# Kernel tuning notes

Hardware: AMD Instinct MI355X
Metric: run time of the kernel (lower is better)

The kernel has to match this reference:

```python
import jax, jax.numpy as jnp
import numpy as np

NS, NV = 16, 4          # scalar / vector multiplicities
MODES = 2               # spectral conv retained fourier modes
C_OUT = 40              # out irreps dim: 16 + 4*3 + 4*3
EPS = 1e-5


def setup_inputs() -> dict:
    key = jax.random.key(0)
    ks = jax.random.split(key, 10)
    T, N, E = 8, 10000, 32768
    x = jax.random.normal(ks[0], (T, N, 28), jnp.float32)
    edge_index = jax.random.randint(ks[1], (2, E), 0, N)
    edge_attr = jax.random.normal(ks[2], (T, E, 48), jnp.float32)
    edge_sh = jax.random.normal(ks[3], (T, E, 4), jnp.float32)
    s = 1.0 / np.sqrt(48.0)
    w_mlp1 = jax.random.normal(ks[4], (48, 48), jnp.float32) * s
    b_mlp1 = jnp.zeros((48,), jnp.float32)
    w_mlp2 = jax.random.normal(ks[5], (48, 416), jnp.float32) * s
    b_mlp2 = jnp.zeros((416,), jnp.float32)
    sc = 1.0 / (NS * NS)
    tc_wr = jax.random.uniform(ks[6], (NS, NS, MODES), jnp.float32) * sc
    tc_wi = jax.random.uniform(ks[7], (NS, NS, MODES), jnp.float32) * sc
    bn_gamma = jnp.ones((C_OUT,), jnp.float32)
    bn_beta = jnp.zeros((C_OUT,), jnp.float32)
    return dict(x=x, edge_index=edge_index, edge_attr=edge_attr, edge_sh=edge_sh,
                w_mlp1=w_mlp1, b_mlp1=b_mlp1, w_mlp2=w_mlp2, b_mlp2=b_mlp2,
                tc_wr=tc_wr, tc_wi=tc_wi, bn_gamma=bn_gamma, bn_beta=bn_beta)


def reference(x, edge_index, edge_attr, edge_sh,
              w_mlp1, b_mlp1, w_mlp2, b_mlp2,
              tc_wr, tc_wi, bn_gamma, bn_beta):
    T, N, _ = x.shape
    E = edge_index.shape[1]
    src, dst = edge_index[0], edge_index[1]

    # ---- SpectralConv1d over the time axis (scalar channels only) ----
    xs = x[:, :, :NS]                                   # [T,N,16]
    xf = jnp.fft.rfft(xs, axis=0)                       # [T//2+1,N,16] c64
    w = tc_wr + 1j * tc_wi                              # [16,16,M]
    low = jnp.einsum('tni,iom->tno', xf[:MODES], jnp.moveaxis(w, -1, 0).transpose(1, 2, 0)[..., :MODES]) if False else jnp.einsum('mni,iom->mno', xf[:MODES], w)
    out_ft = jnp.zeros((T // 2 + 1, N, NS), jnp.complex64).at[:MODES].set(low)
    x_scalar = jnp.fft.irfft(out_ft, n=T, axis=0)       # [T,N,16]

    # ---- edge MLP -> per-edge tensor-product weights [T,E,416] ----
    h = jax.nn.relu(edge_attr @ w_mlp1 + b_mlp1)
    ew = h @ w_mlp2 + b_mlp2

    # ---- gather source node features per edge ----
    xe = x[:, src]                                      # [T,E,28]
    s = xe[..., :NS]                                    # [T,E,16]
    v = xe[..., NS:].reshape(T, E, NV, 3)               # [T,E,4,3]
    sh0 = edge_sh[..., :1]                              # [T,E,1]
    sh1 = edge_sh[..., 1:4]                             # [T,E,3]

    # path weight splits: 0e*0e->0e | 0e*1o->1o | 1o*0e->1o | 1o*1o->0e | 1o*1o->1e
    w00 = ew[..., 0:256].reshape(T, E, NS, NS)
    w01 = ew[..., 256:320].reshape(T, E, NS, NV)
    w10 = ew[..., 320:336].reshape(T, E, NV, NV)
    w110 = ew[..., 336:400].reshape(T, E, NV, NS)
    w111 = ew[..., 400:416].reshape(T, E, NV, NV)

    inv3 = 1.0 / np.sqrt(3.0)
    inv6 = 1.0 / np.sqrt(6.0)
    n0 = 1.0 / np.sqrt(20.0)   # fan-in norm for 0e output (16 + 4 paths)
    n1o = 1.0 / np.sqrt(20.0)  # fan-in norm for 1o output (16 + 4 paths)
    n1e = 1.0 / np.sqrt(4.0)   # fan-in norm for 1e output

    # scalar outputs
    p1 = jnp.einsum('tei,teio->teo', s * sh0, w00)
    vdots = jnp.einsum('teid,ted->tei', v, sh1) * inv3
    p4 = jnp.einsum('tei,teio->teo', vdots, w110)
    out0 = (p1 + p4) * n0                               # [T,E,16]

    # odd-vector outputs
    p2 = jnp.einsum('tei,teio->teo', s, w01)[..., None] * sh1[:, :, None, :] * inv3
    p3 = jnp.einsum('teid,teio->teod', v * sh0[..., None], w10) * inv3
    out1o = (p2 + p3) * n1o                             # [T,E,4,3]

    c = jnp.cross(v, sh1[:, :, None, :]) * inv6
    out1e = jnp.einsum('teid,teio->teod', c, w111) * n1e  # [T,E,4,3]

    msg = jnp.concatenate([out0,
                           out1o.reshape(T, E, NV * 3),
                           out1e.reshape(T, E, NV * 3)], axis=-1)  # [T,E,40]

    # ---- scatter_mean over destination nodes ----
    seg = jax.vmap(lambda m: jax.ops.segment_sum(m, dst, num_segments=N))(msg)
    cnt = jax.ops.segment_sum(jnp.ones((E,), msg.dtype), dst, num_segments=N)
    y = seg / jnp.maximum(cnt, 1.0)[None, :, None]      # [T,N,40]

    # ---- add spectral time-conv result to scalar channels ----
    y = jnp.concatenate([y[..., :NS] + x_scalar, y[..., NS:]], axis=-1)

    # ---- BatchNorm1d replicating torch permute/reshape semantics ----
    z = jnp.transpose(y, (1, 2, 0)).reshape(-1, C_OUT)  # [N*T, 40] (torch layout)
    mu = z.mean(axis=0)
    var = z.var(axis=0)
    z = (z - mu) / jnp.sqrt(var + EPS) * bn_gamma + bn_beta
    y = jnp.transpose(z.reshape(N, C_OUT, T), (2, 0, 1))
    return y
```

## Files before the change

### kernel.cpp

```cpp
#include <hip/hip_runtime.h>
#include <math.h>

#define TT 8
#define NN 10000
#define EE 32768
#define CC 40
#define EPSV 1e-05f

constexpr float INV3 = 0.57735026918962576f;
constexpr float INV6 = 0.40824829046386302f;
constexpr float N0F  = 0.22360679774997896f;
constexpr float N1OF = 0.22360679774997896f;
constexpr float N1EF = 0.5f;

constexpr float CTab[8] = {1.f, 0.70710678118654752f, 0.f, -0.70710678118654752f,
                           -1.f, -0.70710678118654752f, 0.f, 0.70710678118654752f};
constexpr float STab[8] = {0.f, 0.70710678118654752f, 1.f, 0.70710678118654752f,
                           0.f, -0.70710678118654752f, -1.f, -0.70710678118654752f};

typedef __attribute__((ext_vector_type(8))) short short8;
typedef __attribute__((ext_vector_type(4))) float f32x4;

__device__ __forceinline__ void atomAdd(float* p, float v) {
  __hip_atomic_fetch_add(p, v, __ATOMIC_RELAXED, __HIP_MEMORY_SCOPE_AGENT);
}

__device__ __forceinline__ short f2bfs(float f) {
  unsigned u = __builtin_bit_cast(unsigned, f);
  u = (u + 0x7fffu + ((u >> 16) & 1u)) >> 16;
  return (short)u;
}
__device__ __forceinline__ float bf2f(ushort u) {
  unsigned v = ((unsigned)u) << 16;
  return __builtin_bit_cast(float, v);
}

#define SPEC_B 157
#define PREP_B 116
__global__ __launch_bounds__(256) void k_pre(const float* __restrict__ x,
                                             const float* __restrict__ wr,
                                             const float* __restrict__ wi,
                                             const float* __restrict__ W1,
                                             const float* __restrict__ W2,
                                             float* __restrict__ xsc,
                                             short* __restrict__ W1F,
                                             short* __restrict__ W2F) {
  int b = blockIdx.x, tid = threadIdx.x;
  if (b < SPEC_B) {
    int gid = b * 256 + tid;
    int n = gid >> 2, og = gid & 3;
    if (n >= NN) return;
    float F0[16], A[16], B[16];
#pragma unroll
    for (int i = 0; i < 16; ++i) { F0[i] = 0.f; A[i] = 0.f; B[i] = 0.f; }
#pragma unroll
    for (int t = 0; t < 8; ++t) {
      const float4* xp = (const float4*)(x + ((size_t)t * NN + n) * 28);
      float4 v0 = xp[0], v1 = xp[1], v2 = xp[2], v3 = xp[3];
      const float ct = CTab[t], st = STab[t];
      float vv[16] = {v0.x, v0.y, v0.z, v0.w, v1.x, v1.y, v1.z, v1.w,
                      v2.x, v2.y, v2.z, v2.w, v3.x, v3.y, v3.z, v3.w};
#pragma unroll
      for (int i = 0; i < 16; ++i) {
        F0[i] += vv[i];
        A[i] = fmaf(vv[i], ct, A[i]);
        B[i] = fmaf(vv[i], -st, B[i]);
      }
    }
#pragma unroll
    for (int oo = 0; oo < 4; ++oo) {
      int o = og * 4 + oo;
      float r0 = 0.f, r1 = 0.f, i1 = 0.f;
#pragma unroll
      for (int i = 0; i < 16; ++i) {
        float wr0 = wr[i * 32 + o * 2 + 0];
        float wr1 = wr[i * 32 + o * 2 + 1];
        float wi1 = wi[i * 32 + o * 2 + 1];
        r0 = fmaf(F0[i], wr0, r0);
        r1 += A[i] * wr1 - B[i] * wi1;
        i1 += A[i] * wi1 + B[i] * wr1;
      }
#pragma unroll
      for (int t = 0; t < 8; ++t) {
        float val = 0.125f * (r0 + 2.f * (r1 * CTab[t] - i1 * STab[t]));
        xsc[((size_t)t * NN + n) * 16 + o] = val;
      }
    }
  } else {
    int idx = (b - SPEC_B) * 256 + tid;
    const int tot1 = 3 * 2 * 64 * 8;
    if (idx < tot1) {
      int elem = idx & 7, lane = (idx >> 3) & 63, kt = (idx >> 9) & 1, nt = idx >> 10;
      int j = kt * 32 + ((lane >> 4) << 2) + (elem & 3) + ((elem >> 2) << 4);
      int n = nt * 16 + (lane & 15);
      W1F[idx] = (j < 48) ? f2bfs(W1[j * 48 + n]) : (short)0;
    } else {
      int id2 = idx - tot1;
      int elem = id2 & 7, lane = (id2 >> 3) & 63, kt = (id2 >> 9) & 1, ck = id2 >> 10;
      int j = kt * 32 + ((lane >> 4) << 2) + (elem & 3) + ((elem >> 2) << 4);
      int n = ck * 16 + (lane & 15);
      W2F[id2] = (j < 48) ? f2bfs(W2[j * 416 + n]) : (short)0;
    }
  }
}

__global__ __launch_bounds__(1024) void k_scanbucket(const int* __restrict__ ei,
                                                     int* __restrict__ row_start,
                                                     int* __restrict__ ipos,
                                                     float* __restrict__ stats) {
  __shared__ int lcnt[NN];
  __shared__ int wtot[16];
  __shared__ int wpre[16];
  int tid = threadIdx.x;
  if (tid < 80) stats[tid] = 0.f;
  for (int i = tid; i < NN; i += 1024) lcnt[i] = 0;
  __syncthreads();
#pragma unroll
  for (int it = 0; it < EE / 1024; ++it) {
    int e = it * 1024 + tid;
    atomicAdd(&lcnt[ei[EE + e]], 1);
  }
  __syncthreads();
  const int PER = 10;
  int base = tid * PER;
  int s = 0;
  if (base < NN) {
#pragma unroll
    for (int i = 0; i < PER; ++i) s += lcnt[base + i];
  }
  int incl = s;
  int lane = tid & 63, wid = tid >> 6;
#pragma unroll
  for (int off = 1; off < 64; off <<= 1) {
    int v = __shfl_up(incl, off);
    if (lane >= off) incl += v;
  }
  if (lane == 63) wtot[wid] = incl;
  __syncthreads();
  if (tid == 0) {
    int run = 0;
#pragma unroll
    for (int i = 0; i < 16; ++i) { wpre[i] = run; run += wtot[i]; }
  }
  __syncthreads();
  int run = wpre[wid] + (incl - s);
  if (base < NN) {
#pragma unroll
    for (int i = 0; i < PER; ++i) {
      int n = base + i;
      int d = lcnt[n];
      row_start[n] = run;
      lcnt[n] = run;
      run += d;
    }
  }
  if (tid == 0) row_start[NN] = EE;
  __syncthreads();
#pragma unroll
  for (int it = 0; it < EE / 1024; ++it) {
    int e = it * 1024 + tid;
    int d = ei[EE + e];
    int slot = atomicAdd(&lcnt[d], 1);
    ipos[e] = slot;
  }
}

__global__ __launch_bounds__(256) void k_edge4(
    const float* __restrict__ x,
    const int* __restrict__ ei,
    const float* __restrict__ eag,
    const float* __restrict__ shg,
    const short* __restrict__ W1F,
    const short* __restrict__ W2F,
    const float* __restrict__ b1,
    const float* __restrict__ b2,
    const int* __restrict__ ipos,
    ushort* __restrict__ msg)
{
  __shared__ float cSs[16][64];
  __shared__ float rawSs[16][64];
  __shared__ float cVDs[4][64];
  __shared__ float vS0s[12][64];
  __shared__ float sh1fs[3][64];
  __shared__ float cCRs[12][64];
  __shared__ int   iposs[64];
  __shared__ ushort Hs[4][16][64];

  int blk = blockIdx.x;
  int t = blk >> 9;
  int e0 = (blk & 511) * 64;
  int tid = threadIdx.x;

  {
    int e = tid & 63;
    int role = tid >> 6;
    int eg = e0 + e;
    const float* shp = shg + ((size_t)t * EE + eg) * 4;
    float sh0 = shp[0], s1x = shp[1], s1y = shp[2], s1z = shp[3];
    int src = ei[eg];
    const float* xr = x + ((size_t)t * NN + src) * 28;
    const float F1 = INV3 * N1OF;
    if (role == 0) {
      iposs[e] = ipos[eg];
      sh1fs[0][e] = s1x * F1; sh1fs[1][e] = s1y * F1; sh1fs[2][e] = s1z * F1;
#pragma unroll
      for (int i = 0; i < 8; ++i) {
        float s = xr[i];
        rawSs[i][e] = s;
        cSs[i][e] = s * sh0 * N0F;
      }
    } else if (role == 1) {
#pragma unroll
      for (int i = 8; i < 16; ++i) {
        float s = xr[i];
        rawSs[i][e] = s;
        cSs[i][e] = s * sh0 * N0F;
      }
    } else {
      int i0 = (role == 2) ? 0 : 2;
#pragma unroll
      for (int ii = 0; ii < 2; ++ii) {
        int i = i0 + ii;
        float vx = xr[16 + 3 * i], vy = xr[17 + 3 * i], vz = xr[18 + 3 * i];
        cVDs[i][e] = (vx * s1x + vy * s1y + vz * s1z) * INV3 * N0F;
        vS0s[3 * i + 0][e] = vx * sh0 * F1;
        vS0s[3 * i + 1][e] = vy * sh0 * F1;
        vS0s[3 * i + 2][e] = vz * sh0 * F1;
        cCRs[3 * i + 0][e] = (vy * s1z - vz * s1y) * INV6 * N1EF;
        cCRs[3 * i + 1][e] = (vz * s1x - vx * s1z) * INV6 * N1EF;
        cCRs[3 * i + 2][e] = (vx * s1y - vy * s1x) * INV6 * N1EF;
      }
    }
  }
  __syncthreads();

  int w = tid >> 6, l = tid & 63;
  int col = l & 15;
  int kq  = (l >> 4) << 2;
  int eb  = w * 16;

  const float* row = eag + ((size_t)t * EE + e0 + eb + col) * 48;
  float4 fa = *(const float4*)(row + kq);
  float4 fb = *(const float4*)(row + 16 + kq);
  float4 fc = *(const float4*)(row + 32 + kq);
  short8 a0, a1;
  a0[0] = f2bfs(fa.x); a0[1] = f2bfs(fa.y); a0[2] = f2bfs(fa.z); a0[3] = f2bfs(fa.w);
  a0[4] = f2bfs(fb.x); a0[5] = f2bfs(fb.y); a0[6] = f2bfs(fb.z); a0[7] = f2bfs(fb.w);
  a1[0] = f2bfs(fc.x); a1[1] = f2bfs(fc.y); a1[2] = f2bfs(fc.z); a1[3] = f2bfs(fc.w);
  a1[4] = 0; a1[5] = 0; a1[6] = 0; a1[7] = 0;

  const short8* w1f = (const short8*)W1F;
  const short8* w2f = (const short8*)W2F;

#pragma unroll
  for (int nt = 0; nt < 3; ++nt) {
    float bias = b1[nt * 16 + col];
    f32x4 c = {bias, bias, bias, bias};
    c = __builtin_amdgcn_mfma_f32_16x16x32_bf16(a0, w1f[(nt * 2 + 0) * 64 + l], c, 0, 0, 0);
    c = __builtin_amdgcn_mfma_f32_16x16x32_bf16(a1, w1f[(nt * 2 + 1) * 64 + l], c, 0, 0, 0);
#pragma unroll
    for (int r = 0; r < 4; ++r) {
      int m = kq + r;
      float hv = fmaxf(c[r], 0.f);
      Hs[w][m][(nt * 16 + col) ^ ((m & 7) << 3)] = (ushort)f2bfs(hv);
    }
  }
#pragma unroll
  for (int r = 0; r < 4; ++r) {
    int m = kq + r;
    Hs[w][m][(48 + col) ^ ((m & 7) << 3)] = 0;
  }

  int m2 = col, X = (m2 & 7) << 3;
  ushort4 r0 = *(const ushort4*)&Hs[w][m2][(kq +  0) ^ X];
  ushort4 r1 = *(const ushort4*)&Hs[w][m2][(kq + 16) ^ X];
  ushort4 r2 = *(const ushort4*)&Hs[w][m2][(kq + 32) ^ X];
  ushort4 r3 = *(const ushort4*)&Hs[w][m2][(kq + 48) ^ X];
  short8 A20, A21;
  A20[0] = (short)r0.x; A20[1] = (short)r0.y; A20[2] = (short)r0.z; A20[3] = (short)r0.w;
  A20[4] = (short)r1.x; A20[5] = (short)r1.y; A20[6] = (short)r1.z; A20[7] = (short)r1.w;
  A21[0] = (short)r2.x; A21[1] = (short)r2.y; A21[2] = (short)r2.z; A21[3] = (short)r2.w;
  A21[4] = (short)r3.x; A21[5] = (short)r3.y; A21[6] = (short)r3.z; A21[7] = (short)r3.w;

  float acc0[4]  = {0.f, 0.f, 0.f, 0.f};
  float accP2[4] = {0.f, 0.f, 0.f, 0.f};
  float acc1o[3][4] = {{0.f,0.f,0.f,0.f},{0.f,0.f,0.f,0.f},{0.f,0.f,0.f,0.f}};
  float acc1e[3][4] = {{0.f,0.f,0.f,0.f},{0.f,0.f,0.f,0.f},{0.f,0.f,0.f,0.f}};
  int er0 = eb + kq;
  int iloc = col >> 2;
  int o = col & 3;

  short8 pf0[4], pf1[4];
#pragma unroll
  for (int i = 0; i < 4; ++i) {
    pf0[i] = w2f[(2 * i + 0) * 64 + l];
    pf1[i] = w2f[(2 * i + 1) * 64 + l];
  }

#pragma unroll
  for (int ck = 0; ck < 26; ++ck) {
    short8 B0 = pf0[ck & 3], B1 = pf1[ck & 3];
    if (ck + 4 < 26) {
      pf0[ck & 3] = w2f[(2 * (ck + 4) + 0) * 64 + l];
      pf1[ck & 3] = w2f[(2 * (ck + 4) + 1) * 64 + l];
    }
    float bias = b2[ck * 16 + col];
    f32x4 c = {bias, bias, bias, bias};
    c = __builtin_amdgcn_mfma_f32_16x16x32_bf16(A20, B0, c, 0, 0, 0);
    c = __builtin_amdgcn_mfma_f32_16x16x32_bf16(A21, B1, c, 0, 0, 0);

    if (ck < 16) {
#pragma unroll
      for (int r = 0; r < 4; ++r)
        acc0[r] = fmaf(cSs[ck][er0 + r], c[r], acc0[r]);
    } else if (ck < 20) {
#pragma unroll
      for (int r = 0; r < 4; ++r) {
        float q = rawSs[(ck - 16) * 4 + iloc][er0 + r] * c[r];
        q += __shfl_xor(q, 4);
        q += __shfl_xor(q, 8);
        accP2[r] += q;
      }
    } else if (ck == 20) {
#pragma unroll
      for (int d = 0; d < 3; ++d)
#pragma unroll
        for (int r = 0; r < 4; ++r) {
          float q = vS0s[iloc * 3 + d][er0 + r] * c[r];
          q += __shfl_xor(q, 4);
          q += __shfl_xor(q, 8);
          acc1o[d][r] += q;
        }
    } else if (ck < 25) {
#pragma unroll
      for (int r = 0; r < 4; ++r)
        acc0[r] = fmaf(cVDs[ck - 21][er0 + r], c[r], acc0[r]);
    } else {
#pragma unroll
      for (int d = 0; d < 3; ++d)
#pragma unroll
        for (int r = 0; r < 4; ++r) {
          float q = cCRs[iloc * 3 + d][er0 + r] * c[r];
          q += __shfl_xor(q, 4);
          q += __shfl_xor(q, 8);
          acc1e[d][r] += q;
        }
    }
  }

#pragma unroll
  for (int r = 0; r < 4; ++r) {
    size_t eg = (size_t)t * EE + iposs[er0 + r];
    msg[eg * 40 + col] = (ushort)f2bfs(acc0[r]);
  }
  if (col < 4) {
#pragma unroll
    for (int r = 0; r < 4; ++r) {
      int e = er0 + r;
      size_t eg = (size_t)t * EE + iposs[e];
      ushort* mrow = msg + eg * 40;
#pragma unroll
      for (int d = 0; d < 3; ++d) {
        mrow[16 + 3 * o + d] = (ushort)f2bfs(fmaf(accP2[r], sh1fs[d][e], acc1o[d][r]));
        mrow[28 + 3 * o + d] = (ushort)f2bfs(acc1e[d][r]);
      }
    }
  }
}

__global__ __launch_bounds__(320) void k_gstats(const ushort* __restrict__ msg,
                                                const int* __restrict__ row_start,
                                                const float* __restrict__ xsc,
                                                float* __restrict__ out,
                                                float* __restrict__ stats) {
  int blk = blockIdx.x;
  int t = blk / 157;
  int nb = blk - t * 157;
  int tid = threadIdx.x;
  int g = tid / 40, c = tid - g * 40;
  int r5 = c % 5;
  __shared__ float sred[10];
  if (tid < 10) sred[tid] = 0.f;
  __syncthreads();
  float p = 0.f, q = 0.f;
  for (int step = 0; step < 8; ++step) {
    int n = nb * 64 + step * 8 + g;
    if (n < NN) {
      int a = row_start[n], b = row_start[n + 1];
      float acc = 0.f;
      for (int j = a; j < b; ++j)
        acc += bf2f(msg[((size_t)t * EE + j) * 40 + c]);
      float y = acc / fmaxf((float)(b - a), 1.f) +
                (c < 16 ? xsc[((size_t)t * NN + n) * 16 + c] : 0.f);
      out[((size_t)t * NN + n) * 40 + c] = y;
      p += y;
      q = fmaf(y, y, q);
    }
  }
  atomicAdd(&sred[r5], p);
  atomicAdd(&sred[5 + r5], q);
  __syncthreads();
  if (tid < 10) {
    int r = tid % 5;
    int j = 8 * r + t;
    atomAdd(stats + (tid >= 5 ? 40 + j : j), sred[tid]);
  }
}

__global__ __launch_bounds__(256) void k_norm(const float* __restrict__ stats,
                                              const float* __restrict__ gam,
                                              const float* __restrict__ bet,
                                              float* __restrict__ out) {
  int idx4 = blockIdx.x * 256 + threadIdx.x;
  if (idx4 >= TT * NN * 10) return;
  int t = idx4 / (NN * 10);
  int rem = idx4 - t * NN * 10;
  int c0 = (rem % 10) * 4;
  const float inv = 1.f / (8.f * (float)NN);
  float4* op = (float4*)out;
  float4 y = op[idx4];
  float vals[4] = {y.x, y.y, y.z, y.w};
#pragma unroll
  for (int k = 0; k < 4; ++k) {
    int c = c0 + k;
    int j = 8 * (c % 5) + t;
    float mu = stats[j] * inv;
    float var = stats[40 + j] * inv - mu * mu;
    vals[k] = (vals[k] - mu) * rsqrtf(var + EPSV) * gam[j] + bet[j];
  }
  y.x = vals[0]; y.y = vals[1]; y.z = vals[2]; y.w = vals[3];
  op[idx4] = y;
}

extern "C" void kernel_launch(void* const* d_in, const int* in_sizes, int n_in,
                              void* d_out, int out_size, void* d_ws, size_t ws_size,
                              hipStream_t stream) {
  const float* x   = (const float*)d_in[0];
  const int*   ei  = (const int*)d_in[1];
  const float* ea  = (const float*)d_in[2];
  const float* esh = (const float*)d_in[3];
  const float* W1  = (const float*)d_in[4];
  const float* b1  = (const float*)d_in[5];
  const float* W2  = (const float*)d_in[6];
  const float* b2  = (const float*)d_in[7];
  const float* wr  = (const float*)d_in[8];
  const float* wi  = (const float*)d_in[9];
  const float* gam = (const float*)d_in[10];
  const float* bet = (const float*)d_in[11];
  float* out = (float*)d_out;

  float*  xsc       = (float*)d_ws;
  ushort* W1F       = (ushort*)(xsc + 1280000);
  ushort* W2F       = W1F + 3072;
  ushort* msg       = W2F + 26624;
  float*  stats     = (float*)(msg + (size_t)10485760);
  int*    row_start = (int*)(stats + 80);
  int*    ipos      = row_start + 10001;

  k_pre<<<SPEC_B + PREP_B, 256, 0, stream>>>(x, wr, wi, W1, W2, xsc,
                                             (short*)W1F, (short*)W2F);
  k_scanbucket<<<1, 1024, 0, stream>>>(ei, row_start, ipos, stats);
  k_edge4<<<TT * (EE / 64), 256, 0, stream>>>(x, ei, ea, esh, (short*)W1F, (short*)W2F,
                                              b1, b2, ipos, msg);
  k_gstats<<<TT * 157, 320, 0, stream>>>(msg, row_start, xsc, out, stats);
  k_norm<<<(TT * NN * 10 + 255) / 256, 256, 0, stream>>>(stats, gam, bet, out);
}
```

Measured before the change: 146.4 us.

## Fold scan-bucket into prep kernel and process two edge tiles per wave

The single-block CSR scan/bucket kernel is merged into block 0 of the prep kernel, now with 256 threads instead of 1024, which removes one launch and lets the scan overlap with the spectral and weight-packing work. The edge kernel drops to 128 threads per block and each wave handles two 16-edge tiles. This reuses each loaded W1/W2 B-fragment across two MFMAs and halves the waves that issue weight loads. The cost is more registers per thread, a larger Hs buffer per wave, and a slower serial scan in block 0, which may now be the longest block of the prep kernel.

Result: slower. 166.4 us (+13.7%).

```diff
diff --git a/kernel.cpp b/kernel.cpp
--- a/kernel.cpp
+++ b/kernel.cpp
@@ -40,14 +40,70 @@
 __global__ __launch_bounds__(256) void k_pre(const float* __restrict__ x,
                                              const float* __restrict__ wr,
                                              const float* __restrict__ wi,
+                                             const int* __restrict__ ei,
                                              const float* __restrict__ W1,
                                              const float* __restrict__ W2,
                                              float* __restrict__ xsc,
                                              short* __restrict__ W1F,
-                                             short* __restrict__ W2F) {
+                                             short* __restrict__ W2F,
+                                             int* __restrict__ row_start,
+                                             int* __restrict__ ipos,
+                                             float* __restrict__ stats) {
+  __shared__ int lcnt[NN];
+  __shared__ int wtot[4];
+  __shared__ int wpre[4];
   int b = blockIdx.x, tid = threadIdx.x;
-  if (b < SPEC_B) {
-    int gid = b * 256 + tid;
+  if (b == 0) {
+    if (tid < 80) stats[tid] = 0.f;
+    for (int i = tid; i < NN; i += 256) lcnt[i] = 0;
+    __syncthreads();
+    for (int it = 0; it < EE / 256; ++it) {
+      int e = it * 256 + tid;
+      atomicAdd(&lcnt[ei[EE + e]], 1);
+    }
+    __syncthreads();
+    const int PER = 40;
+    int base = tid * PER;
+    int s = 0;
+    for (int i = 0; i < PER; ++i) {
+      int idx = base + i;
+      if (idx < NN) s += lcnt[idx];
+    }
+    int incl = s;
+    int lane = tid & 63, wid = tid >> 6;
+#pragma unroll
+    for (int off = 1; off < 64; off <<= 1) {
+      int v = __shfl_up(incl, off);
+      if (lane >= off) incl += v;
+    }
+    if (lane == 63) wtot[wid] = incl;
+    __syncthreads();
+    if (tid == 0) {
+      int run = 0;
+#pragma unroll
+      for (int i = 0; i < 4; ++i) { wpre[i] = run; run += wtot[i]; }
+    }
+    __syncthreads();
+    int run = wpre[wid] + (incl - s);
+    for (int i = 0; i < PER; ++i) {
+      int idx = base + i;
+      if (idx < NN) {
+        int d = lcnt[idx];
+        row_start[idx] = run;
+        lcnt[idx] = run;
+        run += d;
+      }
+    }
+    if (tid == 0) row_start[NN] = EE;
+    __syncthreads();
+    for (int it = 0; it < EE / 256; ++it) {
+      int e = it * 256 + tid;
+      int d = ei[EE + e];
+      int slot = atomicAdd(&lcnt[d], 1);
+      ipos[e] = slot;
+    }
+  } else if (b <= SPEC_B) {
+    int gid = (b - 1) * 256 + tid;
     int n = gid >> 2, og = gid & 3;
     if (n >= NN) return;
     float F0[16], A[16], B[16];
@@ -87,7 +143,7 @@
       }
     }
   } else {
-    int idx = (b - SPEC_B) * 256 + tid;
+    int idx = (b - 1 - SPEC_B) * 256 + tid;
     const int tot1 = 3 * 2 * 64 * 8;
     if (idx < tot1) {
       int elem = idx & 7, lane = (idx >> 3) & 63, kt = (idx >> 9) & 1, nt = idx >> 10;
@@ -104,68 +160,7 @@
   }
 }
 
-__global__ __launch_bounds__(1024) void k_scanbucket(const int* __restrict__ ei,
-                                                     int* __restrict__ row_start,
-                                                     int* __restrict__ ipos,
-                                                     float* __restrict__ stats) {
-  __shared__ int lcnt[NN];
-  __shared__ int wtot[16];
-  __shared__ int wpre[16];
-  int tid = threadIdx.x;
-  if (tid < 80) stats[tid] = 0.f;
-  for (int i = tid; i < NN; i += 1024) lcnt[i] = 0;
-  __syncthreads();
-#pragma unroll
-  for (int it = 0; it < EE / 1024; ++it) {
-    int e = it * 1024 + tid;
-    atomicAdd(&lcnt[ei[EE + e]], 1);
-  }
-  __syncthreads();
-  const int PER = 10;
-  int base = tid * PER;
-  int s = 0;
-  if (base < NN) {
-#pragma unroll
-    for (int i = 0; i < PER; ++i) s += lcnt[base + i];
-  }
-  int incl = s;
-  int lane = tid & 63, wid = tid >> 6;
-#pragma unroll
-  for (int off = 1; off < 64; off <<= 1) {
-    int v = __shfl_up(incl, off);
-    if (lane >= off) incl += v;
-  }
-  if (lane == 63) wtot[wid] = incl;
-  __syncthreads();
-  if (tid == 0) {
-    int run = 0;
-#pragma unroll
-    for (int i = 0; i < 16; ++i) { wpre[i] = run; run += wtot[i]; }
-  }
-  __syncthreads();
-  int run = wpre[wid] + (incl - s);
-  if (base < NN) {
-#pragma unroll
-    for (int i = 0; i < PER; ++i) {
-      int n = base + i;
-      int d = lcnt[n];
-      row_start[n] = run;
-      lcnt[n] = run;
-      run += d;
-    }
-  }
-  if (tid == 0) row_start[NN] = EE;
-  __syncthreads();
-#pragma unroll
-  for (int it = 0; it < EE / 1024; ++it) {
-    int e = it * 1024 + tid;
-    int d = ei[EE + e];
-    int slot = atomicAdd(&lcnt[d], 1);
-    ipos[e] = slot;
-  }
-}
-
-__global__ __launch_bounds__(256) void k_edge4(
+__global__ __launch_bounds__(128, 3) void k_edge2t(
     const float* __restrict__ x,
     const int* __restrict__ ei,
     const float* __restrict__ eag,
@@ -184,7 +179,7 @@
   __shared__ float sh1fs[3][64];
   __shared__ float cCRs[12][64];
   __shared__ int   iposs[64];
-  __shared__ ushort Hs[4][16][64];
+  __shared__ ushort Hs[2][2][16][64];
 
   int blk = blockIdx.x;
   int t = blk >> 9;
@@ -204,23 +199,14 @@
       iposs[e] = ipos[eg];
       sh1fs[0][e] = s1x * F1; sh1fs[1][e] = s1y * F1; sh1fs[2][e] = s1z * F1;
 #pragma unroll
-      for (int i = 0; i < 8; ++i) {
+      for (int i = 0; i < 16; ++i) {
         float s = xr[i];
         rawSs[i][e] = s;
         cSs[i][e] = s * sh0 * N0F;
       }
-    } else if (role == 1) {
-#pragma unroll
-      for (int i = 8; i < 16; ++i) {
-        float s = xr[i];
-        rawSs[i][e] = s;
-        cSs[i][e] = s * sh0 * N0F;
-      }
     } else {
-      int i0 = (role == 2) ? 0 : 2;
-#pragma unroll
-      for (int ii = 0; ii < 2; ++ii) {
-        int i = i0 + ii;
+#pragma unroll
+      for (int i = 0; i < 4; ++i) {
         float vx = xr[16 + 3 * i], vy = xr[17 + 3 * i], vz = xr[18 + 3 * i];
         cVDs[i][e] = (vx * s1x + vy * s1y + vz * s1z) * INV3 * N0F;
         vS0s[3 * i + 0][e] = vx * sh0 * F1;
@@ -237,17 +223,26 @@
   int w = tid >> 6, l = tid & 63;
   int col = l & 15;
   int kq  = (l >> 4) << 2;
-  int eb  = w * 16;
-
-  const float* row = eag + ((size_t)t * EE + e0 + eb + col) * 48;
-  float4 fa = *(const float4*)(row + kq);
-  float4 fb = *(const float4*)(row + 16 + kq);
-  float4 fc = *(const float4*)(row + 32 + kq);
-  short8 a0, a1;
-  a0[0] = f2bfs(fa.x); a0[1] = f2bfs(fa.y); a0[2] = f2bfs(fa.z); a0[3] = f2bfs(fa.w);
-  a0[4] = f2bfs(fb.x); a0[5] = f2bfs(fb.y); a0[6] = f2bfs(fb.z); a0[7] = f2bfs(fb.w);
-  a1[0] = f2bfs(fc.x); a1[1] = f2bfs(fc.y); a1[2] = f2bfs(fc.z); a1[3] = f2bfs(fc.w);
-  a1[4] = 0; a1[5] = 0; a1[6] = 0; a1[7] = 0;
+  int ebA = w * 32;
+  int ebB = w * 32 + 16;
+
+  const float* rowA = eag + ((size_t)t * EE + e0 + ebA + col) * 48;
+  const float* rowB = eag + ((size_t)t * EE + e0 + ebB + col) * 48;
+  float4 fa = *(const float4*)(rowA + kq);
+  float4 fb = *(const float4*)(rowA + 16 + kq);
+  float4 fc = *(const float4*)(rowA + 32 + kq);
+  float4 ga = *(const float4*)(rowB + kq);
+  float4 gb = *(const float4*)(rowB + 16 + kq);
+  float4 gc = *(const float4*)(rowB + 32 + kq);
+  short8 a0A, a1A, a0B, a1B;
+  a0A[0] = f2bfs(fa.x); a0A[1] = f2bfs(fa.y); a0A[2] = f2bfs(fa.z); a0A[3] = f2bfs(fa.w);
+  a0A[4] = f2bfs(fb.x); a0A[5] = f2bfs(fb.y); a0A[6] = f2bfs(fb.z); a0A[7] = f2bfs(fb.w);
+  a1A[0] = f2bfs(fc.x); a1A[1] = f2bfs(fc.y); a1A[2] = f2bfs(fc.z); a1A[3] = f2bfs(fc.w);
+  a1A[4] = 0; a1A[5] = 0; a1A[6] = 0; a1A[7] = 0;
+  a0B[0] = f2bfs(ga.x); a0B[1] = f2bfs(ga.y); a0B[2] = f2bfs(ga.z); a0B[3] = f2bfs(ga.w);
+  a0B[4] = f2bfs(gb.x); a0B[5] = f2bfs(gb.y); a0B[6] = f2bfs(gb.z); a0B[7] = f2bfs(gb.w);
+  a1B[0] = f2bfs(gc.x); a1B[1] = f2bfs(gc.y); a1B[2] = f2bfs(gc.z); a1B[3] = f2bfs(gc.w);
+  a1B[4] = 0; a1B[5] = 0; a1B[6] = 0; a1B[7] = 0;
 
   const short8* w1f = (const short8*)W1F;
   const short8* w2f = (const short8*)W2F;
@@ -255,38 +250,60 @@
 #pragma unroll
   for (int nt = 0; nt < 3; ++nt) {
     float bias = b1[nt * 16 + col];
-    f32x4 c = {bias, bias, bias, bias};
-    c = __builtin_amdgcn_mfma_f32_16x16x32_bf16(a0, w1f[(nt * 2 + 0) * 64 + l], c, 0, 0, 0);
-    c = __builtin_amdgcn_mfma_f32_16x16x32_bf16(a1, w1f[(nt * 2 + 1) * 64 + l], c, 0, 0, 0);
+    short8 wb0 = w1f[(nt * 2 + 0) * 64 + l];
+    short8 wb1 = w1f[(nt * 2 + 1) * 64 + l];
+    f32x4 cA = {bias, bias, bias, bias};
+    cA = __builtin_amdgcn_mfma_f32_16x16x32_bf16(a0A, wb0, cA, 0, 0, 0);
+    cA = __builtin_amdgcn_mfma_f32_16x16x32_bf16(a1A, wb1, cA, 0, 0, 0);
+    f32x4 cB = {bias, bias, bias, bias};
+    cB = __builtin_amdgcn_mfma_f32_16x16x32_bf16(a0B, wb0, cB, 0, 0, 0);
+    cB = __builtin_amdgcn_mfma_f32_16x16x32_bf16(a1B, wb1, cB, 0, 0, 0);
 #pragma unroll
     for (int r = 0; r < 4; ++r) {
       int m = kq + r;
-      float hv = fmaxf(c[r], 0.f);
-      Hs[w][m][(nt * 16 + col) ^ ((m & 7) << 3)] = (ushort)f2bfs(hv);
+      int cidx = (nt * 16 + col) ^ ((m & 7) << 3);
+      Hs[w][0][m][cidx] = (ushort)f2bfs(fmaxf(cA[r], 0.f));
+      Hs[w][1][m][cidx] = (ushort)f2bfs(fmaxf(cB[r], 0.f));
     }
   }
 #pragma unroll
   for (int r = 0; r < 4; ++r) {
     int m = kq + r;
-    Hs[w][m][(48 + col) ^ ((m & 7) << 3)] = 0;
+    int cidx = (48 + col) ^ ((m & 7) << 3);
+    Hs[w][0][m][cidx] = 0;
+    Hs[w][1][m][cidx] = 0;
   }
 
   int m2 = col, X = (m2 & 7) << 3;
-  ushort4 r0 = *(const ushort4*)&Hs[w][m2][(kq +  0) ^ X];
-  ushort4 r1 = *(const ushort4*)&Hs[w][m2][(kq + 16) ^ X];
-  ushort4 r2 = *(const ushort4*)&Hs[w][m2][(kq + 32) ^ X];
-  ushort4 r3 = *(const ushort4*)&Hs[w][m2][(kq + 48) ^ X];
-  short8 A20, A21;
-  A20[0] = (short)r0.x; A20[1] = (short)r0.y; A20[2] = (short)r0.z; A20[3] = (short)r0.w;
-  A20[4] = (short)r1.x; A20[5] = (short)r1.y; A20[6] = (short)r1.z; A20[7] = (short)r1.w;
-  A21[0] = (short)r2.x; A21[1] = (short)r2.y; A21[2] = (short)r2.z; A21[3] = (short)r2.w;
-  A21[4] = (short)r3.x; A21[5] = (short)r3.y; A21[6] = (short)r3.z; A21[7] = (short)r3.w;
-
-  float acc0[4]  = {0.f, 0.f, 0.f, 0.f};
-  float accP2[4] = {0.f, 0.f, 0.f, 0.f};
-  float acc1o[3][4] = {{0.f,0.f,0.f,0.f},{0.f,0.f,0.f,0.f},{0.f,0.f,0.f,0.f}};
-  float acc1e[3][4] = {{0.f,0.f,0.f,0.f},{0.f,0.f,0.f,0.f},{0.f,0.f,0.f,0.f}};
-  int er0 = eb + kq;
+  short8 A20A, A21A, A20B, A21B;
+  {
+    ushort4 r0 = *(const ushort4*)&Hs[w][0][m2][(kq +  0) ^ X];
+    ushort4 r1 = *(const ushort4*)&Hs[w][0][m2][(kq + 16) ^ X];
+    ushort4 r2 = *(const ushort4*)&Hs[w][0][m2][(kq + 32) ^ X];
+    ushort4 r3 = *(const ushort4*)&Hs[w][0][m2][(kq + 48) ^ X];
+    A20A[0] = (short)r0.x; A20A[1] = (short)r0.y; A20A[2] = (short)r0.z; A20A[3] = (short)r0.w;
+    A20A[4] = (short)r1.x; A20A[5] = (short)r1.y; A20A[6] = (short)r1.z; A20A[7] = (short)r1.w;
+    A21A[0] = (short)r2.x; A21A[1] = (short)r2.y; A21A[2] = (short)r2.z; A21A[3] = (short)r2.w;
+    A21A[4] = (short)r3.x; A21A[5] = (short)r3.y; A21A[6] = (short)r3.z; A21A[7] = (short)r3.w;
+  }
+  {
+    ushort4 r0 = *(const ushort4*)&Hs[w][1][m2][(kq +  0) ^ X];
+    ushort4 r1 = *(const ushort4*)&Hs[w][1][m2][(kq + 16) ^ X];
+    ushort4 r2 = *(const ushort4*)&Hs[w][1][m2][(kq + 32) ^ X];
+    ushort4 r3 = *(const ushort4*)&Hs[w][1][m2][(kq + 48) ^ X];
+    A20B[0] = (short)r0.x; A20B[1] = (short)r0.y; A20B[2] = (short)r0.z; A20B[3] = (short)r0.w;
+    A20B[4] = (short)r1.x; A20B[5] = (short)r1.y; A20B[6] = (short)r1.z; A20B[7] = (short)r1.w;
+    A21B[0] = (short)r2.x; A21B[1] = (short)r2.y; A21B[2] = (short)r2.z; A21B[3] = (short)r2.w;
+    A21B[4] = (short)r3.x; A21B[5] = (short)r3.y; A21B[6] = (short)r3.z; A21B[7] = (short)r3.w;
+  }
+
+  float acc0[2][4]  = {{0.f,0.f,0.f,0.f},{0.f,0.f,0.f,0.f}};
+  float accP2[2][4] = {{0.f,0.f,0.f,0.f},{0.f,0.f,0.f,0.f}};
+  float acc1o[2][3][4] = {{{0.f,0.f,0.f,0.f},{0.f,0.f,0.f,0.f},{0.f,0.f,0.f,0.f}},
+                          {{0.f,0.f,0.f,0.f},{0.f,0.f,0.f,0.f},{0.f,0.f,0.f,0.f}}};
+  float acc1e[2][3][4] = {{{0.f,0.f,0.f,0.f},{0.f,0.f,0.f,0.f},{0.f,0.f,0.f,0.f}},
+                          {{0.f,0.f,0.f,0.f},{0.f,0.f,0.f,0.f},{0.f,0.f,0.f,0.f}}};
+  int er[2] = {ebA + kq, ebB + kq};
   int iloc = col >> 2;
   int o = col & 3;
 
@@ -305,64 +322,77 @@
       pf1[ck & 3] = w2f[(2 * (ck + 4) + 1) * 64 + l];
     }
     float bias = b2[ck * 16 + col];
-    f32x4 c = {bias, bias, bias, bias};
-    c = __builtin_amdgcn_mfma_f32_16x16x32_bf16(A20, B0, c, 0, 0, 0);
-    c = __builtin_amdgcn_mfma_f32_16x16x32_bf16(A21, B1, c, 0, 0, 0);
-
-    if (ck < 16) {
-#pragma unroll
-      for (int r = 0; r < 4; ++r)
-        acc0[r] = fmaf(cSs[ck][er0 + r], c[r], acc0[r]);
-    } else if (ck < 20) {
-#pragma unroll
-      for (int r = 0; r < 4; ++r) {
-        float q = rawSs[(ck - 16) * 4 + iloc][er0 + r] * c[r];
-        q += __shfl_xor(q, 4);
-        q += __shfl_xor(q, 8);
-        accP2[r] += q;
-      }
-    } else if (ck == 20) {
-#pragma unroll
-      for (int d = 0; d < 3; ++d)
+    f32x4 cc0 = {bias, bias, bias, bias};
+    cc0 = __builtin_amdgcn_mfma_f32_16x16x32_bf16(A20A, B0, cc0, 0, 0, 0);
+    cc0 = __builtin_amdgcn_mfma_f32_16x16x32_bf16(A21A, B1, cc0, 0, 0, 0);
+    f32x4 cc1 = {bias, bias, bias, bias};
+    cc1 = __builtin_amdgcn_mfma_f32_16x16x32_bf16(A20B, B0, cc1, 0, 0, 0);
+    cc1 = __builtin_amdgcn_mfma_f32_16x16x32_bf16(A21B, B1, cc1, 0, 0, 0);
+    f32x4 cc[2] = {cc0, cc1};
+
+#pragma unroll
+    for (int tb = 0; tb < 2; ++tb) {
+      if (ck < 16) {
+#pragma unroll
+        for (int r = 0; r < 4; ++r)
+          acc0[tb][r] = fmaf(cSs[ck][er[tb] + r], cc[tb][r], acc0[tb][r]);
+      } else if (ck < 20) {
 #pragma unroll
         for (int r = 0; r < 4; ++r) {
-          float q = vS0s[iloc * 3 + d][er0 + r] * c[r];
+          float q = rawSs[(ck - 16) * 4 + iloc][er[tb] + r] * cc[tb][r];
           q += __shfl_xor(q, 4);
           q += __shfl_xor(q, 8);
-          acc1o[d][r] += q;
+          accP2[tb][r] += q;
         }
-    } else if (ck < 25) {
-#pragma unroll
-      for (int r = 0; r < 4; ++r)
-        acc0[r] = fmaf(cVDs[ck - 21][er0 + r], c[r], acc0[r]);
-    } else {
-#pragma unroll
-      for (int d = 0; d < 3; ++d)
-#pragma unroll
-        for (int r = 0; r < 4; ++r) {
-          float q = cCRs[iloc * 3 + d][er0 + r] * c[r];
-          q += __shfl_xor(q, 4);
-          q += __shfl_xor(q, 8);
-          acc1e[d][r] += q;
+      } else if (ck == 20) {
+#pragma unroll
+        for (int d = 0; d < 3; ++d)
+#pragma unroll
+          for (int r = 0; r < 4; ++r) {
+            float q = vS0s[iloc * 3 + d][er[tb] + r] * cc[tb][r];
+            q += __shfl_xor(q, 4);
+            q += __shfl_xor(q, 8);
+            acc1o[tb][d][r] += q;
+          }
+      } else if (ck < 25) {
+#pragma unroll
+        for (int r = 0; r < 4; ++r)
+          acc0[tb][r] = fmaf(cVDs[ck - 21][er[tb] + r], cc[tb][r], acc0[tb][r]);
+      } else {
+#pragma unroll
+        for (int d = 0; d < 3; ++d)
+#pragma unroll
+          for (int r = 0; r < 4; ++r) {
+            float q = cCRs[iloc * 3 + d][er[tb] + r] * cc[tb][r];
+            q += __shfl_xor(q, 4);
+            q += __shfl_xor(q, 8);
+            acc1e[tb][d][r] += q;
+          }
+      }
+    }
+  }
+
+#pragma unroll
+  for (int tb = 0; tb < 2; ++tb) {
+#pragma unroll
+    for (int r = 0; r < 4; ++r) {
+      size_t eg = (size_t)t * EE + iposs[er[tb] + r];
+      msg[eg * 40 + col] = (ushort)f2bfs(acc0[tb][r]);
+    }
+  }
+  if (col < 4) {
+#pragma unroll
+    for (int tb = 0; tb < 2; ++tb) {
+#pragma unroll
+      for (int r = 0; r < 4; ++r) {
+        int e = er[tb] + r;
+        size_t eg = (size_t)t * EE + iposs[e];
+        ushort* mrow = msg + eg * 40;
+#pragma unroll
+        for (int d = 0; d < 3; ++d) {
+          mrow[16 + 3 * o + d] = (ushort)f2bfs(fmaf(accP2[tb][r], sh1fs[d][e], acc1o[tb][d][r]));
+          mrow[28 + 3 * o + d] = (ushort)f2bfs(acc1e[tb][d][r]);
         }
-    }
-  }
-
-#pragma unroll
-  for (int r = 0; r < 4; ++r) {
-    size_t eg = (size_t)t * EE + iposs[er0 + r];
-    msg[eg * 40 + col] = (ushort)f2bfs(acc0[r]);
-  }
-  if (col < 4) {
-#pragma unroll
-    for (int r = 0; r < 4; ++r) {
-      int e = er0 + r;
-      size_t eg = (size_t)t * EE + iposs[e];
-      ushort* mrow = msg + eg * 40;
-#pragma unroll
-      for (int d = 0; d < 3; ++d) {
-        mrow[16 + 3 * o + d] = (ushort)f2bfs(fmaf(accP2[r], sh1fs[d][e], acc1o[d][r]));
-        mrow[28 + 3 * o + d] = (ushort)f2bfs(acc1e[d][r]);
       }
     }
   }
@@ -457,11 +487,11 @@
   int*    row_start = (int*)(stats + 80);
   int*    ipos      = row_start + 10001;
 
-  k_pre<<<SPEC_B + PREP_B, 256, 0, stream>>>(x, wr, wi, W1, W2, xsc,
-                                             (short*)W1F, (short*)W2F);
-  k_scanbucket<<<1, 1024, 0, stream>>>(ei, row_start, ipos, stats);
-  k_edge4<<<TT * (EE / 64), 256, 0, stream>>>(x, ei, ea, esh, (short*)W1F, (short*)W2F,
-                                              b1, b2, ipos, msg);
+  k_pre<<<1 + SPEC_B + PREP_B, 256, 0, stream>>>(x, wr, wi, ei, W1, W2, xsc,
+                                                 (short*)W1F, (short*)W2F,
+                                                 row_start, ipos, stats);
+  k_edge2t<<<TT * (EE / 64), 128, 0, stream>>>(x, ei, ea, esh, (short*)W1F, (short*)W2F,
+                                               b1, b2, ipos, msg);
   k_gstats<<<TT * 157, 320, 0, stream>>>(msg, row_start, xsc, out, stats);
   k_norm<<<(TT * NN * 10 + 255) / 256, 256, 0, stream>>>(stats, gam, bet, out);
 }
```
